# Optimization experiments

Measured on AMD Instinct MI355X. Metric: run time of the kernel, lower is better.

Reference implementation:

```python
import jax, jax.numpy as jnp
import numpy as np

TOP_K = 2

def setup_inputs() -> dict:
    key = jax.random.key(0)
    ks = jax.random.split(key, 8)
    B, S, D = 2, 2048, 1024
    N_r, N_s = 16, 2
    u = jax.random.normal(ks[0], (B, S, D), dtype=jnp.float32)
    centroids = jax.random.normal(ks[1], (N_r, D), dtype=jnp.float32)
    expert_biases = jnp.zeros((N_r,), dtype=jnp.float32)
    # routed expert Linear params: y = u @ W.T + b, W stored [E, d_out, d_in]
    Wr = jax.random.normal(ks[2], (N_r, D, D), dtype=jnp.float32) * (1.0 / np.sqrt(D))
    br = jax.random.normal(ks[3], (N_r, D), dtype=jnp.float32) * 0.01
    Ws = jax.random.normal(ks[4], (N_s, D, D), dtype=jnp.float32) * (1.0 / np.sqrt(D))
    bs = jax.random.normal(ks[5], (N_s, D), dtype=jnp.float32) * 0.01
    return {"u": u, "centroids": centroids, "expert_biases": expert_biases,
            "Wr": Wr, "br": br, "Ws": Ws, "bs": bs}

def reference(u, centroids, expert_biases, Wr, br, Ws, bs):
    N_r = centroids.shape[0]
    N_s = Ws.shape[0]
    # routing scores over experts
    raw_scores = jnp.einsum('bsd,ed->bse', u, centroids)          # [B,S,E]
    s = jax.nn.softmax(raw_scores + expert_biases, axis=-1)
    # scatter top-k softmax values (un-renormalized, as in the source) into gates
    topk_vals, topk_idx = jax.lax.top_k(s, TOP_K)                  # [B,S,K]
    g_topk = jnp.sum(jax.nn.one_hot(topk_idx, N_r, dtype=s.dtype) * topk_vals[..., None], axis=-2)  # [B,S,E]
    # dense per-expert Linear for all tokens, then gated combine (faithful to source)
    xe = jnp.einsum('bsd,eod->bseo', u, Wr) + br                   # [B,S,E,D]
    routed = jnp.einsum('bse,bseo->bso', g_topk, xe)               # [B,S,D]
    # shared experts: mean of N_s dense Linears
    shared = (jnp.einsum('bsd,eod->bso', u, Ws) + jnp.sum(bs, axis=0)) / N_s
    return u + routed + shared
```

## Files before the change

### kernel.cpp

```cpp
#include <hip/hip_runtime.h>

typedef unsigned short u16x8 __attribute__((ext_vector_type(8)));
typedef short          s16x8 __attribute__((ext_vector_type(8)));
typedef float          f32x4 __attribute__((ext_vector_type(4)));

#define NTOK   4096
#define DMODEL 1024
#define NEXP   16
#define TOPK   2
#define BK     32
#define NK     (DMODEL / BK)
#define MAXT   128

__device__ inline unsigned short f2bf(float f) {
    unsigned int x = __float_as_uint(f);
    x += 0x7fffu + ((x >> 16) & 1u);
    return (unsigned short)(x >> 16);
}
__device__ inline float bf2f(unsigned short h) {
    unsigned int x = ((unsigned int)h) << 16;
    return __uint_as_float(x);
}

__device__ inline void gld16(const void* g, void* l) {
    __builtin_amdgcn_global_load_lds(
        (const __attribute__((address_space(1))) void*)g,
        (__attribute__((address_space(3))) void*)l, 16, 0, 0);
}

#define NWR8  (NEXP * DMODEL * DMODEL / 8)
#define NWS8  (DMODEL * DMODEL / 8)
#define NB8   ((NEXP + 1) * DMODEL / 8)
#define RBLK  (NTOK / 4)
#define CBLK  ((NWR8 + NWS8 + NB8 + 255) / 256)

__global__ void prep_kernel(const float* __restrict__ u,
                            const float* __restrict__ cent,
                            const float* __restrict__ ebias,
                            const float* __restrict__ Wr,
                            const float* __restrict__ br,
                            const float* __restrict__ Ws,
                            const float* __restrict__ bs,
                            unsigned short* __restrict__ ub,
                            unsigned short* __restrict__ w17,
                            float* __restrict__ b17,
                            float* __restrict__ topk_g,
                            int*   __restrict__ topk_i) {
    int bid = blockIdx.x;
    if (bid >= RBLK) {
        int id = (bid - RBLK) * 256 + threadIdx.x;
        if (id < NWR8) {
            size_t base = (size_t)id * 8;
            f32x4 a = *(const f32x4*)&Wr[base];
            f32x4 b = *(const f32x4*)&Wr[base + 4];
            u16x8 o;
#pragma unroll
            for (int i = 0; i < 4; i++) { o[i] = f2bf(a[i]); o[i + 4] = f2bf(b[i]); }
            *(u16x8*)&w17[base] = o;
        } else if (id < NWR8 + NWS8) {
            size_t base = (size_t)(id - NWR8) * 8;
            f32x4 a0 = *(const f32x4*)&Ws[base];
            f32x4 b0 = *(const f32x4*)&Ws[base + 4];
            f32x4 a1 = *(const f32x4*)&Ws[(size_t)DMODEL * DMODEL + base];
            f32x4 b1 = *(const f32x4*)&Ws[(size_t)DMODEL * DMODEL + base + 4];
            u16x8 o;
#pragma unroll
            for (int i = 0; i < 4; i++) {
                o[i]     = f2bf(a0[i] + a1[i]);
                o[i + 4] = f2bf(b0[i] + b1[i]);
            }
            *(u16x8*)&w17[(size_t)NEXP * DMODEL * DMODEL + base] = o;
        } else if (id < NWR8 + NWS8 + NB8) {
            int base = (id - NWR8 - NWS8) * 8;
#pragma unroll
            for (int i = 0; i < 8; i++) {
                int idx = base + i;
                b17[idx] = idx < NEXP * DMODEL
                    ? br[idx]
                    : bs[idx - NEXP * DMODEL] + bs[idx - NEXP * DMODEL + DMODEL];
            }
        }
        return;
    }
    int wid  = threadIdx.x >> 6;
    int lane = threadIdx.x & 63;
    int t = bid * 4 + wid;
    const float* urow = u + (size_t)t * DMODEL;

    double acc[NEXP];
#pragma unroll
    for (int e = 0; e < NEXP; e++) acc[e] = 0.0;

    for (int j = 0; j < DMODEL / 64; j++) {
        int d = j * 64 + lane;
        float uf = urow[d];
        ub[(size_t)t * DMODEL + d] = f2bf(uf);
        double uv = (double)uf;
#pragma unroll
        for (int e = 0; e < NEXP; e++)
            acc[e] += uv * (double)cent[e * DMODEL + d];
    }
#pragma unroll
    for (int e = 0; e < NEXP; e++) {
        for (int off = 32; off; off >>= 1)
            acc[e] += __shfl_xor(acc[e], off);
    }
    if (lane == 0) {
        double mx = -1e300;
#pragma unroll
        for (int e = 0; e < NEXP; e++) {
            acc[e] += (double)ebias[e];
            if (acc[e] > mx) mx = acc[e];
        }
        double ex[NEXP], den = 0.0;
#pragma unroll
        for (int e = 0; e < NEXP; e++) { ex[e] = exp(acc[e] - mx); den += ex[e]; }
        int i1 = -1, i2 = -1;
        double v1 = -1.0, v2 = -1.0;
        for (int e = 0; e < NEXP; e++) {
            double v = ex[e];
            if (v > v1)      { v2 = v1; i2 = i1; v1 = v; i1 = e; }
            else if (v > v2) { v2 = v;  i2 = e; }
        }
        topk_g[t * 2 + 0] = (float)(v1 / den);
        topk_g[t * 2 + 1] = (float)(v2 / den);
        topk_i[t * 2 + 0] = i1;
        topk_i[t * 2 + 1] = i2;
    }
}

__global__ void bucket16(const float* __restrict__ tg,
                         const int*   __restrict__ ti,
                         int* __restrict__ cnt,
                         int* __restrict__ tokL,
                         float* __restrict__ gateL,
                         int* __restrict__ idL) {
    int e = blockIdx.x;
    __shared__ int base;
    if (threadIdx.x == 0) base = 0;
    __syncthreads();
    int lane = threadIdx.x & 63;
    for (int c0 = 0; c0 < NTOK * TOPK; c0 += 256) {
        int id = c0 + threadIdx.x;
        bool m = (ti[id] == e);
        unsigned long long mask = __ballot(m);
        int wcnt = __popcll(mask);
        int wpos = 0;
        if (lane == 0) wpos = atomicAdd(&base, wcnt);
        wpos = __shfl(wpos, 0);
        if (m) {
            int pos = wpos + __popcll(mask & ((1ull << lane) - 1ull));
            tokL[e * NTOK + pos]  = id >> 1;
            gateL[e * NTOK + pos] = tg[id];
            idL[e * NTOK + pos]   = id;
        }
    }
    __syncthreads();
    if (threadIdx.x == 0) cnt[e] = base;
}

__global__ __launch_bounds__(128, 2)
void moe_gemm(const unsigned short* __restrict__ ub,
              const unsigned short* __restrict__ w17,
              const float* __restrict__ b17,
              const int*   __restrict__ cnt,
              const int*   __restrict__ tokL,
              const float* __restrict__ gateL,
              const int*   __restrict__ idL,
              const float* __restrict__ u,
              float* __restrict__ out,
              unsigned short* __restrict__ y) {
    int bid = blockIdx.x;
    int tile = bid >> 3;
    int n0 = (bid & 7) * 128;
    int e, row0;
    if (tile < NTOK / 128) {
        e = NEXP; row0 = tile << 7;
    } else {
        int rt = tile - NTOK / 128;
        int ee = 0;
        for (; ee < NEXP; ee++) {
            int nt = (cnt[ee] + 127) >> 7;
            if (rt < nt) break;
            rt -= nt;
        }
        if (ee >= NEXP) return;
        e = ee; row0 = rt << 7;
    }
    bool is_shared = (e == NEXP);
    int count = is_shared ? NTOK : cnt[e];

    __shared__ __align__(16) unsigned short As[2][128 * BK];
    __shared__ __align__(16) unsigned short Bs[2][128 * BK];

    int t = threadIdx.x;
    int lane = t & 63, wid = t >> 6;
    int lr = lane & 15, lk4 = lane >> 4;
    int rchunk = (lk4 ^ ((lr >> 1) & 3)) * 8;

    int srow = lane >> 2;
    int scs  = ((lane & 3) ^ ((lane >> 3) & 3)) * 8;

    const int* tl = tokL + e * NTOK;
    const unsigned short* asrc[4];
    const unsigned short* bsrc[4];
    const unsigned short* bb = w17 + (size_t)e * DMODEL * DMODEL + (size_t)n0 * DMODEL;
#pragma unroll
    for (int p = 0; p < 4; p++) {
        int gi = row0 + wid * 64 + p * 16 + srow;
        int tok = is_shared ? gi : tl[gi < count ? gi : count - 1];
        asrc[p] = ub + (size_t)tok * DMODEL + scs;
        bsrc[p] = bb + (size_t)(wid * 64 + p * 16 + srow) * DMODEL + scs;
    }

#define STAGE(buf, kt) do {                                                     \
    int _k0 = (kt) * BK;                                                        \
    _Pragma("unroll")                                                           \
    for (int p = 0; p < 4; p++) {                                               \
        int r = wid * 64 + p * 16;                                              \
        gld16(asrc[p] + _k0, &As[buf][r * BK]);                                 \
        gld16(bsrc[p] + _k0, &Bs[buf][r * BK]);                                 \
    } } while (0)

    f32x4 acc[8][4];
#pragma unroll
    for (int i = 0; i < 8; i++)
#pragma unroll
        for (int j = 0; j < 4; j++)
#pragma unroll
            for (int v = 0; v < 4; v++) acc[i][j][v] = 0.0f;

    STAGE(0, 0);
    int cur = 0;
    for (int kt = 0; kt < NK; kt++) {
        if (kt + 1 < NK) {
            STAGE(cur ^ 1, kt + 1);
            asm volatile("s_waitcnt vmcnt(8)" ::: "memory");
        } else {
            asm volatile("s_waitcnt vmcnt(0)" ::: "memory");
        }
        __builtin_amdgcn_s_barrier();

        __builtin_amdgcn_s_setprio(1);
        s16x8 b[4];
#pragma unroll
        for (int j = 0; j < 4; j++)
            b[j] = *(const s16x8*)&Bs[cur][(wid * 64 + j * 16 + lr) * BK + rchunk];
#pragma unroll
        for (int i = 0; i < 8; i++) {
            s16x8 a = *(const s16x8*)&As[cur][(i * 16 + lr) * BK + rchunk];
#pragma unroll
            for (int j = 0; j < 4; j++)
                acc[i][j] = __builtin_amdgcn_mfma_f32_16x16x32_bf16(a, b[j], acc[i][j], 0, 0, 0);
        }
        __builtin_amdgcn_s_setprio(0);

        asm volatile("" ::: "memory");
        __builtin_amdgcn_s_barrier();
        cur ^= 1;
    }
#undef STAGE

    const float* be = b17 + e * DMODEL;
    if (is_shared) {
#pragma unroll
        for (int i = 0; i < 8; i++) {
#pragma unroll
            for (int v = 0; v < 4; v++) {
                int row = row0 + i * 16 + lk4 * 4 + v;
#pragma unroll
                for (int j = 0; j < 4; j++) {
                    int col = n0 + wid * 64 + j * 16 + lr;
                    size_t idx = (size_t)row * DMODEL + col;
                    out[idx] = u[idx] + 0.5f * (acc[i][j][v] + be[col]);
                }
            }
        }
    } else {
#pragma unroll
        for (int i = 0; i < 8; i++) {
#pragma unroll
            for (int v = 0; v < 4; v++) {
                int gi = row0 + i * 16 + lk4 * 4 + v;
                if (gi < count) {
                    int id = idL[e * NTOK + gi];
                    float g = gateL[e * NTOK + gi];
                    unsigned short* yr = y + (size_t)id * DMODEL;
#pragma unroll
                    for (int j = 0; j < 4; j++) {
                        int col = n0 + wid * 64 + j * 16 + lr;
                        yr[col] = f2bf(g * (acc[i][j][v] + be[col]));
                    }
                }
            }
        }
    }
}

__global__ void combine_kernel(const unsigned short* __restrict__ y,
                               float* __restrict__ out) {
    int idx = blockIdx.x * 256 + threadIdx.x;
    int tk = idx >> 7;
    int d8 = (idx & 127) * 8;
    size_t base = (size_t)tk * DMODEL + d8;
    u16x8 a = *(const u16x8*)&y[(size_t)(tk * 2) * DMODEL + d8];
    u16x8 b = *(const u16x8*)&y[(size_t)(tk * 2 + 1) * DMODEL + d8];
    f32x4 o0 = *(const f32x4*)&out[base];
    f32x4 o1 = *(const f32x4*)&out[base + 4];
#pragma unroll
    for (int v = 0; v < 4; v++) {
        o0[v] += bf2f(a[v]) + bf2f(b[v]);
        o1[v] += bf2f(a[v + 4]) + bf2f(b[v + 4]);
    }
    *(f32x4*)&out[base] = o0;
    *(f32x4*)&out[base + 4] = o1;
}

extern "C" void kernel_launch(void* const* d_in, const int* in_sizes, int n_in,
                              void* d_out, int out_size, void* d_ws, size_t ws_size,
                              hipStream_t stream) {
    const float* u    = (const float*)d_in[0];
    const float* cent = (const float*)d_in[1];
    const float* eb   = (const float*)d_in[2];
    const float* Wr   = (const float*)d_in[3];
    const float* br   = (const float*)d_in[4];
    const float* Ws   = (const float*)d_in[5];
    const float* bs   = (const float*)d_in[6];
    float* out = (float*)d_out;

    char* ws = (char*)d_ws;
    size_t off = 0;
    auto take = [&](size_t b) { size_t o = off; off += (b + 255) & ~(size_t)255; return o; };
    float* topk_g = (float*)(ws + take(NTOK * TOPK * 4));
    int*   topk_i = (int*)  (ws + take(NTOK * TOPK * 4));
    int*   cnt    = (int*)  (ws + take(64 * 4));
    int*   tokL   = (int*)  (ws + take((size_t)NEXP * NTOK * 4));
    float* gateL  = (float*)(ws + take((size_t)NEXP * NTOK * 4));
    int*   idL    = (int*)  (ws + take((size_t)NEXP * NTOK * 4));
    float* b17    = (float*)(ws + take((size_t)(NEXP + 1) * DMODEL * 4));
    unsigned short* ub  = (unsigned short*)(ws + take((size_t)NTOK * DMODEL * 2));
    unsigned short* w17 = (unsigned short*)(ws + take((size_t)(NEXP + 1) * DMODEL * DMODEL * 2));
    unsigned short* y   = (unsigned short*)(ws + take((size_t)NTOK * TOPK * DMODEL * 2));

    prep_kernel<<<RBLK + CBLK, 256, 0, stream>>>(
        u, cent, eb, Wr, br, Ws, bs, ub, w17, b17, topk_g, topk_i);
    bucket16<<<NEXP, 256, 0, stream>>>(topk_g, topk_i, cnt, tokL, gateL, idL);
    moe_gemm<<<8 * MAXT, 128, 0, stream>>>(
        ub, w17, b17, cnt, tokL, gateL, idL, u, out, y);
    combine_kernel<<<(NTOK * DMODEL / 8) / 256, 256, 0, stream>>>(y, out);
}
```

Measured before the change: 118.2 us.

## Load B tiles directly to registers and use 4-wave 2x2 warp tiling

Reworks the grouped MoE GEMM to launch 256 threads per block arranged as a 2x2 wave grid, each wave computing a 64x64 sub-tile instead of 128x64. The weight (B) operand is no longer staged through LDS; each lane loads its MFMA fragment straight from global memory into registers with double-buffered register sets, while A stays in double-buffered LDS. This removes the B shared-memory traffic and halves LDS use, aiming for higher occupancy and better latency hiding. In exchange, B fragments are fetched per wave with less coalescing, and the hand-placed vmcnt waits must match the exact load ordering.

```diff
diff --git a/kernel.cpp b/kernel.cpp
--- a/kernel.cpp
+++ b/kernel.cpp
@@ -159,7 +159,7 @@
     if (threadIdx.x == 0) cnt[e] = base;
 }
 
-__global__ __launch_bounds__(128, 2)
+__global__ __launch_bounds__(256, 3)
 void moe_gemm(const unsigned short* __restrict__ ub,
               const unsigned short* __restrict__ w17,
               const float* __restrict__ b17,
@@ -191,10 +191,10 @@
     int count = is_shared ? NTOK : cnt[e];
 
     __shared__ __align__(16) unsigned short As[2][128 * BK];
-    __shared__ __align__(16) unsigned short Bs[2][128 * BK];
 
     int t = threadIdx.x;
     int lane = t & 63, wid = t >> 6;
+    int wm = wid >> 1, wn = wid & 1;
     int lr = lane & 15, lk4 = lane >> 4;
     int rchunk = (lk4 ^ ((lr >> 1) & 3)) * 8;
 
@@ -202,75 +202,92 @@
     int scs  = ((lane & 3) ^ ((lane >> 3) & 3)) * 8;
 
     const int* tl = tokL + e * NTOK;
-    const unsigned short* asrc[4];
-    const unsigned short* bsrc[4];
-    const unsigned short* bb = w17 + (size_t)e * DMODEL * DMODEL + (size_t)n0 * DMODEL;
-#pragma unroll
-    for (int p = 0; p < 4; p++) {
-        int gi = row0 + wid * 64 + p * 16 + srow;
+    const unsigned short* asrc[2];
+#pragma unroll
+    for (int p = 0; p < 2; p++) {
+        int gi = row0 + wid * 32 + p * 16 + srow;
         int tok = is_shared ? gi : tl[gi < count ? gi : count - 1];
         asrc[p] = ub + (size_t)tok * DMODEL + scs;
-        bsrc[p] = bb + (size_t)(wid * 64 + p * 16 + srow) * DMODEL + scs;
-    }
-
-#define STAGE(buf, kt) do {                                                     \
-    int _k0 = (kt) * BK;                                                        \
-    _Pragma("unroll")                                                           \
-    for (int p = 0; p < 4; p++) {                                               \
-        int r = wid * 64 + p * 16;                                              \
-        gld16(asrc[p] + _k0, &As[buf][r * BK]);                                 \
-        gld16(bsrc[p] + _k0, &Bs[buf][r * BK]);                                 \
+    }
+    const unsigned short* bb = w17 + (size_t)e * DMODEL * DMODEL + (size_t)n0 * DMODEL;
+    const unsigned short* bp[4];
+#pragma unroll
+    for (int j = 0; j < 4; j++)
+        bp[j] = bb + (size_t)(wn * 64 + j * 16 + lr) * DMODEL + lk4 * 8;
+
+#define STAGE_A(buf, kt) do {                                               \
+    int _k0 = (kt) * BK;                                                    \
+    _Pragma("unroll")                                                       \
+    for (int p = 0; p < 2; p++) {                                           \
+        int r = wid * 32 + p * 16;                                          \
+        gld16(asrc[p] + _k0, &As[buf][r * BK]);                             \
     } } while (0)
 
-    f32x4 acc[8][4];
-#pragma unroll
-    for (int i = 0; i < 8; i++)
+#define LOADB(dstarr, kt) do {                                              \
+    _Pragma("unroll")                                                       \
+    for (int j = 0; j < 4; j++) {                                           \
+        asm volatile("global_load_dwordx4 %0, %1, off"                      \
+                     : "=v"(dstarr[j]) : "v"(bp[j] + (kt) * BK) : "memory");\
+    } } while (0)
+
+#define PHASE(CBUF, NBUF, BC, BN, KT) do {                                  \
+    if ((KT) + 1 < NK) {                                                    \
+        STAGE_A(NBUF, (KT) + 1);                                            \
+        LOADB(BN, (KT) + 1);                                                \
+        asm volatile("s_waitcnt vmcnt(6)" ::: "memory");                    \
+    } else {                                                                \
+        asm volatile("s_waitcnt vmcnt(0)" ::: "memory");                    \
+    }                                                                       \
+    __builtin_amdgcn_sched_barrier(0);                                      \
+    __builtin_amdgcn_s_setprio(1);                                          \
+    _Pragma("unroll")                                                       \
+    for (int i = 0; i < 4; i++) {                                           \
+        s16x8 a = *(const s16x8*)&As[CBUF][(wm * 64 + i * 16 + lr) * BK + rchunk]; \
+        _Pragma("unroll")                                                   \
+        for (int j = 0; j < 4; j++)                                         \
+            acc[i][j] = __builtin_amdgcn_mfma_f32_16x16x32_bf16(a, BC[j], acc[i][j], 0, 0, 0); \
+    }                                                                       \
+    __builtin_amdgcn_s_setprio(0);                                          \
+    if ((KT) + 1 < NK) asm volatile("s_waitcnt vmcnt(4)" ::: "memory");     \
+    __builtin_amdgcn_sched_barrier(0);                                      \
+    __builtin_amdgcn_s_barrier();                                           \
+} while (0)
+
+    f32x4 acc[4][4];
+#pragma unroll
+    for (int i = 0; i < 4; i++)
 #pragma unroll
         for (int j = 0; j < 4; j++)
 #pragma unroll
             for (int v = 0; v < 4; v++) acc[i][j][v] = 0.0f;
 
-    STAGE(0, 0);
-    int cur = 0;
-    for (int kt = 0; kt < NK; kt++) {
-        if (kt + 1 < NK) {
-            STAGE(cur ^ 1, kt + 1);
-            asm volatile("s_waitcnt vmcnt(8)" ::: "memory");
-        } else {
-            asm volatile("s_waitcnt vmcnt(0)" ::: "memory");
-        }
-        __builtin_amdgcn_s_barrier();
-
-        __builtin_amdgcn_s_setprio(1);
-        s16x8 b[4];
-#pragma unroll
-        for (int j = 0; j < 4; j++)
-            b[j] = *(const s16x8*)&Bs[cur][(wid * 64 + j * 16 + lr) * BK + rchunk];
-#pragma unroll
-        for (int i = 0; i < 8; i++) {
-            s16x8 a = *(const s16x8*)&As[cur][(i * 16 + lr) * BK + rchunk];
-#pragma unroll
-            for (int j = 0; j < 4; j++)
-                acc[i][j] = __builtin_amdgcn_mfma_f32_16x16x32_bf16(a, b[j], acc[i][j], 0, 0, 0);
-        }
-        __builtin_amdgcn_s_setprio(0);
-
-        asm volatile("" ::: "memory");
-        __builtin_amdgcn_s_barrier();
-        cur ^= 1;
-    }
-#undef STAGE
+    s16x8 bregA[4], bregB[4];
+
+    STAGE_A(0, 0);
+    LOADB(bregA, 0);
+    asm volatile("s_waitcnt vmcnt(4)" ::: "memory");
+    __builtin_amdgcn_sched_barrier(0);
+    __builtin_amdgcn_s_barrier();
+
+#pragma unroll 1
+    for (int kt = 0; kt < NK; kt += 2) {
+        PHASE(0, 1, bregA, bregB, kt);
+        PHASE(1, 0, bregB, bregA, kt + 1);
+    }
+#undef PHASE
+#undef LOADB
+#undef STAGE_A
 
     const float* be = b17 + e * DMODEL;
     if (is_shared) {
 #pragma unroll
-        for (int i = 0; i < 8; i++) {
+        for (int i = 0; i < 4; i++) {
 #pragma unroll
             for (int v = 0; v < 4; v++) {
-                int row = row0 + i * 16 + lk4 * 4 + v;
+                int row = row0 + wm * 64 + i * 16 + lk4 * 4 + v;
 #pragma unroll
                 for (int j = 0; j < 4; j++) {
-                    int col = n0 + wid * 64 + j * 16 + lr;
+                    int col = n0 + wn * 64 + j * 16 + lr;
                     size_t idx = (size_t)row * DMODEL + col;
                     out[idx] = u[idx] + 0.5f * (acc[i][j][v] + be[col]);
                 }
@@ -278,17 +295,17 @@
         }
     } else {
 #pragma unroll
-        for (int i = 0; i < 8; i++) {
+        for (int i = 0; i < 4; i++) {
 #pragma unroll
             for (int v = 0; v < 4; v++) {
-                int gi = row0 + i * 16 + lk4 * 4 + v;
+                int gi = row0 + wm * 64 + i * 16 + lk4 * 4 + v;
                 if (gi < count) {
                     int id = idL[e * NTOK + gi];
                     float g = gateL[e * NTOK + gi];
                     unsigned short* yr = y + (size_t)id * DMODEL;
 #pragma unroll
                     for (int j = 0; j < 4; j++) {
-                        int col = n0 + wid * 64 + j * 16 + lr;
+                        int col = n0 + wn * 64 + j * 16 + lr;
                         yr[col] = f2bf(g * (acc[i][j][v] + be[col]));
                     }
                 }
@@ -345,7 +362,7 @@
     prep_kernel<<<RBLK + CBLK, 256, 0, stream>>>(
         u, cent, eb, Wr, br, Ws, bs, ub, w17, b17, topk_g, topk_i);
     bucket16<<<NEXP, 256, 0, stream>>>(topk_g, topk_i, cnt, tokL, gateL, idL);
-    moe_gemm<<<8 * MAXT, 128, 0, stream>>>(
+    moe_gemm<<<8 * MAXT, 256, 0, stream>>>(
         ub, w17, b17, cnt, tokL, gateL, idL, u, out, y);
     combine_kernel<<<(NTOK * DMODEL / 8) / 256, 256, 0, stream>>>(y, out);
 }
```

After: 136.7 us. +15.6%, slower.
